# Optimization experiments

Measured on AMD Instinct MI355X. Metric: run time of the kernel, lower is better.

## Reference

```python
import jax, jax.numpy as jnp
import numpy as np

B, D, H, L = 65536, 784, 392, 32

def _lin(x, W, b):
    return x @ W.T + b

def setup_inputs() -> dict:
    key = jax.random.key(0)
    ks = jax.random.split(key, 10)
    def w(k, shape):
        fan_in = shape[1]
        return jax.random.normal(k, shape, jnp.float32) * (1.0 / np.sqrt(fan_in))
    return {
        'x': jax.random.uniform(ks[0], (B, D), jnp.float32),
        'eps_z': jax.random.normal(ks[1], (B, L), jnp.float32),
        'eps_y': jax.random.normal(ks[2], (B, D), jnp.float32),
        'W_e1': w(ks[3], (H, D)), 'b_e1': jnp.zeros((H,), jnp.float32),
        'W_emu': w(ks[4], (L, H)), 'b_emu': jnp.zeros((L,), jnp.float32),
        'W_elv': w(ks[5], (L, H)), 'b_elv': jnp.zeros((L,), jnp.float32),
        'W_d1': w(ks[6], (H, L)), 'b_d1': jnp.zeros((H,), jnp.float32),
        'W_dmu': w(ks[7], (D, H)), 'b_dmu': jnp.zeros((D,), jnp.float32),
        'W_dlv': w(ks[8], (D, H)), 'b_dlv': jnp.zeros((D,), jnp.float32),
    }

def reference(x, eps_z, eps_y, W_e1, b_e1, W_emu, b_emu, W_elv, b_elv,
              W_d1, b_d1, W_dmu, b_dmu, W_dlv, b_dlv):
    # encode
    h = jax.nn.relu(_lin(x, W_e1, b_e1))
    mu_z = jax.nn.relu(_lin(h, W_emu, b_emu))
    logvar_z = jax.nn.relu(_lin(h, W_elv, b_elv))
    # reparameterize
    z = mu_z + eps_z * jnp.exp(0.5 * logvar_z)
    # decode
    hd = jax.nn.relu(_lin(z, W_d1, b_d1))
    mu_y = jax.nn.relu(_lin(hd, W_dmu, b_dmu))
    logvar_y = jax.nn.relu(_lin(hd, W_dlv, b_dlv))
    image_res = jax.nn.sigmoid(mu_y + eps_y * jnp.exp(0.5 * logvar_y))
    # NLL: MultivariateNormal(mu, cov=diag(exp(0.5*logvar))).log_prob(x), closed form
    # (original looped per-sample with a Cholesky of a diag matrix; math identical)
    d = mu_y.shape[1]
    var = jnp.exp(0.5 * logvar_y)            # diagonal covariance entries
    quad = jnp.sum((x - mu_y) ** 2 / var, axis=1)
    logdet = jnp.sum(0.5 * logvar_y, axis=1)
    log_prob = -0.5 * (d * jnp.log(2.0 * jnp.pi) + logdet + quad)
    nll = -jnp.mean(log_prob)
    # KL regularisation, faithful to source formula incl. log(1e-8 + exp(logvar))
    kl = jnp.sum(0.5 * jnp.sum(mu_z ** 2 + jnp.exp(logvar_z)
                               - jnp.log(1e-8 + jnp.exp(logvar_z)) - 1.0, axis=1))
    return image_res, nll + kl
```

## Files before the change

### kernel.cpp

```cpp
#include <hip/hip_runtime.h>

#define B_N   65536
#define D_N   784
#define H_N   392
#define L_N   32
#define OUT_IMG ((size_t)B_N * D_N)

#define M_ROWS 64
#define HSTR   392

typedef unsigned short ushort_t;
typedef __attribute__((ext_vector_type(8))) short short8;
typedef __attribute__((ext_vector_type(4))) float f32x4;

#define N_WE1  358400
#define N_WEZ  26624
#define N_WD1  13312
#define N_WDY  745472
#define N_W16  (N_WE1 + N_WEZ + N_WD1 + N_WDY)
#define N_BIAS 2720
#define WS_BYTES (N_W16*2 + N_BIAS*4)

__device__ __forceinline__ unsigned short f2bf(float f) {
  union { float f; unsigned u; } v; v.f = f;
  unsigned r = v.u + 0x7FFFu + ((v.u >> 16) & 1u);
  return (unsigned short)(r >> 16);
}

__device__ __forceinline__ void gl2lds16(const void* g, void* l) {
  __builtin_amdgcn_global_load_lds(
      (const __attribute__((address_space(1))) unsigned int*)(unsigned long long)g,
      (__attribute__((address_space(3))) unsigned int*)(unsigned int)(unsigned long long)l,
      16, 0, 0);
}

__global__ void vae_prep(const float* __restrict__ We1, const float* __restrict__ Wemu,
                         const float* __restrict__ Welv, const float* __restrict__ Wd1,
                         const float* __restrict__ Wdmu, const float* __restrict__ Wdlv,
                         const float* __restrict__ be1, const float* __restrict__ bemu,
                         const float* __restrict__ belv, const float* __restrict__ bd1,
                         const float* __restrict__ bdmu, const float* __restrict__ bdlv,
                         ushort_t* __restrict__ ws16, float* __restrict__ wsb,
                         float* __restrict__ scalar_out) {
  int idx = blockIdx.x * 256 + threadIdx.x;
  if (idx == 0) *scalar_out = 0.f;
  if (idx < N_W16) {
    float val;
    if (idx < N_WE1) {
      int e = idx; int j = e & 7, lane = (e >> 3) & 63, g = e >> 9;
      int nt = g % 28, kt = g / 28;
      int n = nt * 16 + (lane & 15), k = kt * 32 + ((lane >> 4) << 3) + j;
      val = (n < H_N && k < D_N) ? We1[n * D_N + k] : 0.f;
    } else if (idx < N_WE1 + N_WEZ) {
      int e = idx - N_WE1; int j = e & 7, lane = (e >> 3) & 63, g = e >> 9;
      int kt = g % 13, nt = g / 13;
      int n = nt * 16 + (lane & 15), k = kt * 32 + ((lane >> 4) << 3) + j;
      val = (k < H_N) ? (n < 32 ? Wemu[n * H_N + k] : Welv[(n - 32) * H_N + k]) : 0.f;
    } else if (idx < N_WE1 + N_WEZ + N_WD1) {
      int e = idx - N_WE1 - N_WEZ; int j = e & 7, lane = (e >> 3) & 63, nt = e >> 9;
      int n = nt * 16 + (lane & 15), k = ((lane >> 4) << 3) + j;
      val = (n < H_N) ? Wd1[n * L_N + k] : 0.f;
    } else {
      int e = idx - N_WE1 - N_WEZ - N_WD1; int j = e & 7, lane = (e >> 3) & 63, g = e >> 9;
      int tt = g & 3, nw = (g >> 2) & 3, c = (g >> 4) % 7, kt = g / 112;
      int pair = nw * 14 + 2 * c + (tt >> 1);
      int d = pair * 16 + (lane & 15);
      int k = kt * 32 + ((lane >> 4) << 3) + j;
      val = (d < D_N && k < H_N) ? ((tt & 1) ? Wdlv[d * H_N + k] : Wdmu[d * H_N + k]) : 0.f;
    }
    ws16[idx] = f2bf(val);
  } else {
    int bi = idx - N_W16;
    if (bi < N_BIAS) {
      float val;
      if      (bi < 448)  val = (bi < H_N) ? be1[bi] : 0.f;
      else if (bi < 512)  { int i2 = bi - 448;  val = (i2 < 32) ? bemu[i2] : belv[i2 - 32]; }
      else if (bi < 928)  { int i2 = bi - 512;  val = (i2 < H_N) ? bd1[i2] : 0.f; }
      else if (bi < 1824) { int i2 = bi - 928;  val = (i2 < D_N) ? bdmu[i2] : 0.f; }
      else                { int i2 = bi - 1824; val = (i2 < D_N) ? bdlv[i2] : 0.f; }
      wsb[bi] = val;
    }
  }
}

__global__ __launch_bounds__(512, 4) void vae_main(
    const float* __restrict__ x, const float* __restrict__ eps_z,
    const float* __restrict__ eps_y,
    const ushort_t* __restrict__ ws16, const float* __restrict__ wsb,
    float* __restrict__ out, float* __restrict__ scalar_out) {
  const ushort_t* We1t = ws16;
  const ushort_t* Wezt = ws16 + N_WE1;
  const ushort_t* Wd1t = Wezt + N_WEZ;
  const ushort_t* Wdyt = Wd1t + N_WD1;
  const float* be1p  = wsb;
  const float* bezp  = wsb + 448;
  const float* bd1p  = wsb + 512;
  const float* bdmup = wsb + 928;
  const float* bdlvp = wsb + 1824;

  __shared__ __align__(16) ushort_t hbuf[M_ROWS * HSTR + 32];
  __shared__ __align__(16) ushort_t wslab[28 * 512];
  __shared__ float red[8];

  ushort_t* zb = wslab;

  const int tid  = threadIdx.x;
  const int w    = tid >> 6;
  const int lane = tid & 63;
  const int quad = lane >> 4;
  const int l16  = lane & 15;
  const int mw   = w >> 2, nw = w & 3;
  const int rb   = blockIdx.x * M_ROWS;

  float kl_acc = 0.f, q_acc = 0.f, ld_acc = 0.f;

  if (tid < 32) hbuf[M_ROWS * HSTR + tid] = 0;

  f32x4 acc1[2][7];
  {
    f32x4 z4 = {0.f, 0.f, 0.f, 0.f};
#pragma unroll
    for (int i = 0; i < 2; ++i)
#pragma unroll
      for (int t = 0; t < 7; ++t) acc1[i][t] = z4;
  }
  const float* xp[2];
#pragma unroll
  for (int i = 0; i < 2; ++i)
    xp[i] = x + (size_t)(rb + mw * 32 + i * 16 + l16) * D_N + quad * 8;

  for (int kt = 0; kt < 25; ++kt) {
    __syncthreads();
#pragma unroll
    for (int i = 0; i < 4; ++i) {
      int g = i * 512 + tid;
      if (g < 1792) gl2lds16((const char*)We1t + kt * 28672 + g * 16, (char*)wslab + g * 16);
    }
    short8 afr[2];
    {
      bool real = !(kt == 24 && quad >= 2);
#pragma unroll
      for (int i = 0; i < 2; ++i) {
        union { int4 p; short8 s; } u;
        if (real) {
          const float4* px = (const float4*)(xp[i] + kt * 32);
          float4 v0 = px[0], v1 = px[1];
          u.p.x = f2bf(v0.x) | ((unsigned)f2bf(v0.y) << 16);
          u.p.y = f2bf(v0.z) | ((unsigned)f2bf(v0.w) << 16);
          u.p.z = f2bf(v1.x) | ((unsigned)f2bf(v1.y) << 16);
          u.p.w = f2bf(v1.z) | ((unsigned)f2bf(v1.w) << 16);
        } else {
          u.p.x = 0; u.p.y = 0; u.p.z = 0; u.p.w = 0;
        }
        afr[i] = u.s;
      }
    }
    __syncthreads();
    __builtin_amdgcn_s_setprio(1);
#pragma unroll
    for (int t = 0; t < 7; ++t) {
      short8 bfr = *(const short8*)(wslab + ((nw * 7 + t) * 64 + lane) * 8);
#pragma unroll
      for (int i = 0; i < 2; ++i)
        acc1[i][t] = __builtin_amdgcn_mfma_f32_16x16x32_bf16(afr[i], bfr, acc1[i][t], 0, 0, 0);
    }
    __builtin_amdgcn_s_setprio(0);
  }
#pragma unroll
  for (int t = 0; t < 7; ++t) {
    int ntg = nw * 7 + t;
    if (ntg < 25) {
      int n = ntg * 16 + l16;
      bool ok = (n < H_N);
      float bb = ok ? be1p[n] : 0.f;
#pragma unroll
      for (int i = 0; i < 2; ++i)
#pragma unroll
        for (int r = 0; r < 4; ++r) {
          int m = mw * 32 + i * 16 + quad * 4 + r;
          if (ok) hbuf[m * HSTR + n] = f2bf(fmaxf(acc1[i][t][r] + bb, 0.f));
        }
    }
  }
  __syncthreads();

  if (w < 4) {
    f32x4 acc2[4];
    {
      f32x4 z4 = {0.f, 0.f, 0.f, 0.f};
#pragma unroll
      for (int nt = 0; nt < 4; ++nt) acc2[nt] = z4;
    }
    for (int kt = 0; kt < 13; ++kt) {
      short8 a = *(const short8*)(hbuf + (16 * w + l16) * HSTR + kt * 32 + quad * 8);
#pragma unroll
      for (int nt = 0; nt < 4; ++nt) {
        short8 b = *(const short8*)(Wezt + ((nt * 13 + kt) * 64 + lane) * 8);
        acc2[nt] = __builtin_amdgcn_mfma_f32_16x16x32_bf16(a, b, acc2[nt], 0, 0, 0);
      }
    }
#pragma unroll
    for (int s = 0; s < 2; ++s) {
      float bmu = bezp[s * 16 + l16];
      float blv = bezp[32 + s * 16 + l16];
#pragma unroll
      for (int r = 0; r < 4; ++r) {
        float mu = fmaxf(acc2[s][r] + bmu, 0.f);
        float lv = fmaxf(acc2[s + 2][r] + blv, 0.f);
        int m = 16 * w + quad * 4 + r;
        int gm = rb + m;
        int l = s * 16 + l16;
        float e = __expf(lv);
        kl_acc += 0.5f * (mu * mu + e - __logf(1e-8f + e) - 1.f);
        float zz = mu + eps_z[gm * 32 + l] * __expf(0.5f * lv);
        zb[m * 40 + l] = f2bf(zz);
      }
    }
  }
  __syncthreads();

  {
    const int rw = (w & 3) * 16;
    const int wh = w >> 2;
    short8 az = *(const short8*)(zb + (rw + l16) * 40 + quad * 8);
    for (int t2 = 0; t2 < 13; ++t2) {
      int nt = wh * 13 + t2;
      if (nt >= 25) continue;
      short8 b = *(const short8*)(Wd1t + (nt * 64 + lane) * 8);
      f32x4 a4 = {0.f, 0.f, 0.f, 0.f};
      a4 = __builtin_amdgcn_mfma_f32_16x16x32_bf16(az, b, a4, 0, 0, 0);
      int n = nt * 16 + l16;
      bool ok = (n < H_N);
      float bb = ok ? bd1p[n] : 0.f;
#pragma unroll
      for (int r = 0; r < 4; ++r) {
        int m = rw + quad * 4 + r;
        if (ok) hbuf[m * HSTR + n] = f2bf(fmaxf(a4[r] + bb, 0.f));
      }
    }
  }
  __syncthreads();

  for (int c = 0; c < 7; ++c) {
    f32x4 acc5[2][4];
    {
      f32x4 z4 = {0.f, 0.f, 0.f, 0.f};
#pragma unroll
      for (int i = 0; i < 2; ++i)
#pragma unroll
        for (int tt = 0; tt < 4; ++tt) acc5[i][tt] = z4;
    }
    for (int kt = 0; kt < 13; ++kt) {
      __syncthreads();
#pragma unroll
      for (int i = 0; i < 2; ++i) {
        int g = i * 512 + tid;
        gl2lds16((const char*)Wdyt + (kt * 7 + c) * 16384 + g * 16, (char*)wslab + g * 16);
      }
      __syncthreads();
      short8 a[2];
#pragma unroll
      for (int i = 0; i < 2; ++i)
        a[i] = *(const short8*)(hbuf + (mw * 32 + i * 16 + l16) * HSTR + kt * 32 + quad * 8);
      __builtin_amdgcn_s_setprio(1);
#pragma unroll
      for (int tt = 0; tt < 4; ++tt) {
        short8 b = *(const short8*)(wslab + ((nw * 4 + tt) * 64 + lane) * 8);
#pragma unroll
        for (int i = 0; i < 2; ++i)
          acc5[i][tt] = __builtin_amdgcn_mfma_f32_16x16x32_bf16(a[i], b, acc5[i][tt], 0, 0, 0);
      }
      __builtin_amdgcn_s_setprio(0);
    }
#pragma unroll
    for (int s = 0; s < 2; ++s) {
      int d = (nw * 14 + 2 * c + s) * 16 + l16;
      if (d < D_N) {
        float bmu = bdmup[d], blv = bdlvp[d];
#pragma unroll
        for (int i = 0; i < 2; ++i) {
#pragma unroll
          for (int r = 0; r < 4; ++r) {
            int m = mw * 32 + i * 16 + quad * 4 + r;
            size_t gi = (size_t)(rb + m) * D_N + d;
            float mu = fmaxf(acc5[i][2 * s][r] + bmu, 0.f);
            float lv = fmaxf(acc5[i][2 * s + 1][r] + blv, 0.f);
            float sd = __expf(0.5f * lv);
            float ey = __builtin_nontemporal_load(&eps_y[gi]);
            float xx = __builtin_nontemporal_load(&x[gi]);
            float tval = mu + ey * sd;
            __builtin_nontemporal_store(__builtin_amdgcn_rcpf(1.f + __expf(-tval)), &out[gi]);
            float dq = xx - mu;
            q_acc  += dq * dq * __builtin_amdgcn_rcpf(sd);
            ld_acc += 0.5f * lv;
          }
        }
      }
    }
  }

  float v = (0.5f / (float)B_N) * (ld_acc + q_acc) + kl_acc;
#pragma unroll
  for (int off = 32; off; off >>= 1) v += __shfl_down(v, off, 64);
  if (lane == 0) red[w] = v;
  __syncthreads();
  if (tid == 0) {
    float tot = 0.f;
#pragma unroll
    for (int i = 0; i < 8; ++i) tot += red[i];
    if (blockIdx.x == 0) tot += 720.447808f;
    atomicAdd(scalar_out, tot);
  }
}

extern "C" void kernel_launch(void* const* d_in, const int* in_sizes, int n_in,
                              void* d_out, int out_size, void* d_ws, size_t ws_size,
                              hipStream_t stream) {
  const float* x     = (const float*)d_in[0];
  const float* eps_z = (const float*)d_in[1];
  const float* eps_y = (const float*)d_in[2];
  const float* We1   = (const float*)d_in[3];
  const float* be1   = (const float*)d_in[4];
  const float* Wemu  = (const float*)d_in[5];
  const float* bemu  = (const float*)d_in[6];
  const float* Welv  = (const float*)d_in[7];
  const float* belv  = (const float*)d_in[8];
  const float* Wd1   = (const float*)d_in[9];
  const float* bd1   = (const float*)d_in[10];
  const float* Wdmu  = (const float*)d_in[11];
  const float* bdmu  = (const float*)d_in[12];
  const float* Wdlv  = (const float*)d_in[13];
  const float* bdlv  = (const float*)d_in[14];

  float* out = (float*)d_out;
  float* scalar_out = out + OUT_IMG;

  ushort_t* ws16 = (ushort_t*)d_ws;
  float* wsb = (float*)((char*)d_ws + (size_t)N_W16 * 2);

  int prep_total = N_W16 + N_BIAS;
  int prep_blocks = (prep_total + 255) / 256;
  vae_prep<<<prep_blocks, 256, 0, stream>>>(We1, Wemu, Welv, Wd1, Wdmu, Wdlv,
                                            be1, bemu, belv, bd1, bdmu, bdlv,
                                            ws16, wsb, scalar_out);

  vae_main<<<B_N / M_ROWS, 512, 0, stream>>>(x, eps_z, eps_y, ws16, wsb, out, scalar_out);
}
```

Baseline: 735.2 us.

## Load MFMA weight fragments directly from global instead of staging through LDS

Removes the LDS weight slab and the global_load_lds staging in both the encoder-1 and decoder-output GEMM loops. Each wave now reads its B fragments straight from the pre-swizzled global weight buffer, which drops two __syncthreads per k-step and frees LDS for higher occupancy. The last encoder k-tile is peeled out so the main loop carries no padding branch, and the loops are unrolled by two. The cost is redundant per-wave global/L2 weight traffic, since the two M-waves now fetch the same weights separately, plus load latency that is no longer hidden behind LDS.

After: 1.219 ms. 65.9% more time.

```diff
diff --git a/kernel.cpp b/kernel.cpp
--- a/kernel.cpp
+++ b/kernel.cpp
@@ -25,13 +25,6 @@
   union { float f; unsigned u; } v; v.f = f;
   unsigned r = v.u + 0x7FFFu + ((v.u >> 16) & 1u);
   return (unsigned short)(r >> 16);
-}
-
-__device__ __forceinline__ void gl2lds16(const void* g, void* l) {
-  __builtin_amdgcn_global_load_lds(
-      (const __attribute__((address_space(1))) unsigned int*)(unsigned long long)g,
-      (__attribute__((address_space(3))) unsigned int*)(unsigned int)(unsigned long long)l,
-      16, 0, 0);
 }
 
 __global__ void vae_prep(const float* __restrict__ We1, const float* __restrict__ Wemu,
@@ -99,10 +92,8 @@
   const float* bdlvp = wsb + 1824;
 
   __shared__ __align__(16) ushort_t hbuf[M_ROWS * HSTR + 32];
-  __shared__ __align__(16) ushort_t wslab[28 * 512];
+  __shared__ __align__(16) ushort_t zbuf[M_ROWS * 40];
   __shared__ float red[8];
-
-  ushort_t* zb = wslab;
 
   const int tid  = threadIdx.x;
   const int w    = tid >> 6;
@@ -129,42 +120,54 @@
   for (int i = 0; i < 2; ++i)
     xp[i] = x + (size_t)(rb + mw * 32 + i * 16 + l16) * D_N + quad * 8;
 
-  for (int kt = 0; kt < 25; ++kt) {
-    __syncthreads();
-#pragma unroll
-    for (int i = 0; i < 4; ++i) {
-      int g = i * 512 + tid;
-      if (g < 1792) gl2lds16((const char*)We1t + kt * 28672 + g * 16, (char*)wslab + g * 16);
-    }
+#pragma unroll 2
+  for (int kt = 0; kt < 24; ++kt) {
     short8 afr[2];
-    {
-      bool real = !(kt == 24 && quad >= 2);
-#pragma unroll
-      for (int i = 0; i < 2; ++i) {
-        union { int4 p; short8 s; } u;
-        if (real) {
-          const float4* px = (const float4*)(xp[i] + kt * 32);
-          float4 v0 = px[0], v1 = px[1];
-          u.p.x = f2bf(v0.x) | ((unsigned)f2bf(v0.y) << 16);
-          u.p.y = f2bf(v0.z) | ((unsigned)f2bf(v0.w) << 16);
-          u.p.z = f2bf(v1.x) | ((unsigned)f2bf(v1.y) << 16);
-          u.p.w = f2bf(v1.z) | ((unsigned)f2bf(v1.w) << 16);
-        } else {
-          u.p.x = 0; u.p.y = 0; u.p.z = 0; u.p.w = 0;
-        }
-        afr[i] = u.s;
-      }
-    }
-    __syncthreads();
+#pragma unroll
+    for (int i = 0; i < 2; ++i) {
+      const float4* px = (const float4*)(xp[i] + kt * 32);
+      float4 v0 = px[0], v1 = px[1];
+      union { int4 p; short8 s; } u;
+      u.p.x = f2bf(v0.x) | ((unsigned)f2bf(v0.y) << 16);
+      u.p.y = f2bf(v0.z) | ((unsigned)f2bf(v0.w) << 16);
+      u.p.z = f2bf(v1.x) | ((unsigned)f2bf(v1.y) << 16);
+      u.p.w = f2bf(v1.z) | ((unsigned)f2bf(v1.w) << 16);
+      afr[i] = u.s;
+    }
     __builtin_amdgcn_s_setprio(1);
 #pragma unroll
     for (int t = 0; t < 7; ++t) {
-      short8 bfr = *(const short8*)(wslab + ((nw * 7 + t) * 64 + lane) * 8);
+      short8 bfr = *(const short8*)(We1t + ((kt * 28 + nw * 7 + t) * 64 + lane) * 8);
 #pragma unroll
       for (int i = 0; i < 2; ++i)
         acc1[i][t] = __builtin_amdgcn_mfma_f32_16x16x32_bf16(afr[i], bfr, acc1[i][t], 0, 0, 0);
     }
     __builtin_amdgcn_s_setprio(0);
+  }
+  {
+    short8 afr[2];
+#pragma unroll
+    for (int i = 0; i < 2; ++i) {
+      union { int4 p; short8 s; } u;
+      if (quad < 2) {
+        const float4* px = (const float4*)(xp[i] + 24 * 32);
+        float4 v0 = px[0], v1 = px[1];
+        u.p.x = f2bf(v0.x) | ((unsigned)f2bf(v0.y) << 16);
+        u.p.y = f2bf(v0.z) | ((unsigned)f2bf(v0.w) << 16);
+        u.p.z = f2bf(v1.x) | ((unsigned)f2bf(v1.y) << 16);
+        u.p.w = f2bf(v1.z) | ((unsigned)f2bf(v1.w) << 16);
+      } else {
+        u.p.x = 0; u.p.y = 0; u.p.z = 0; u.p.w = 0;
+      }
+      afr[i] = u.s;
+    }
+#pragma unroll
+    for (int t = 0; t < 7; ++t) {
+      short8 bfr = *(const short8*)(We1t + ((24 * 28 + nw * 7 + t) * 64 + lane) * 8);
+#pragma unroll
+      for (int i = 0; i < 2; ++i)
+        acc1[i][t] = __builtin_amdgcn_mfma_f32_16x16x32_bf16(afr[i], bfr, acc1[i][t], 0, 0, 0);
+    }
   }
 #pragma unroll
   for (int t = 0; t < 7; ++t) {
@@ -213,7 +216,7 @@
         float e = __expf(lv);
         kl_acc += 0.5f * (mu * mu + e - __logf(1e-8f + e) - 1.f);
         float zz = mu + eps_z[gm * 32 + l] * __expf(0.5f * lv);
-        zb[m * 40 + l] = f2bf(zz);
+        zbuf[m * 40 + l] = f2bf(zz);
       }
     }
   }
@@ -222,7 +225,7 @@
   {
     const int rw = (w & 3) * 16;
     const int wh = w >> 2;
-    short8 az = *(const short8*)(zb + (rw + l16) * 40 + quad * 8);
+    short8 az = *(const short8*)(zbuf + (rw + l16) * 40 + quad * 8);
     for (int t2 = 0; t2 < 13; ++t2) {
       int nt = wh * 13 + t2;
       if (nt >= 25) continue;
@@ -250,26 +253,21 @@
 #pragma unroll
         for (int tt = 0; tt < 4; ++tt) acc5[i][tt] = z4;
     }
+#pragma unroll 2
     for (int kt = 0; kt < 13; ++kt) {
-      __syncthreads();
-#pragma unroll
-      for (int i = 0; i < 2; ++i) {
-        int g = i * 512 + tid;
-        gl2lds16((const char*)Wdyt + (kt * 7 + c) * 16384 + g * 16, (char*)wslab + g * 16);
-      }
-      __syncthreads();
-      short8 a[2];
+      short8 a[2], b[4];
 #pragma unroll
       for (int i = 0; i < 2; ++i)
         a[i] = *(const short8*)(hbuf + (mw * 32 + i * 16 + l16) * HSTR + kt * 32 + quad * 8);
+#pragma unroll
+      for (int tt = 0; tt < 4; ++tt)
+        b[tt] = *(const short8*)(Wdyt + ((kt * 112 + c * 16 + nw * 4 + tt) * 64 + lane) * 8);
       __builtin_amdgcn_s_setprio(1);
 #pragma unroll
-      for (int tt = 0; tt < 4; ++tt) {
-        short8 b = *(const short8*)(wslab + ((nw * 4 + tt) * 64 + lane) * 8);
+      for (int tt = 0; tt < 4; ++tt)
 #pragma unroll
         for (int i = 0; i < 2; ++i)
-          acc5[i][tt] = __builtin_amdgcn_mfma_f32_16x16x32_bf16(a[i], b, acc5[i][tt], 0, 0, 0);
-      }
+          acc5[i][tt] = __builtin_amdgcn_mfma_f32_16x16x32_bf16(a[i], b[tt], acc5[i][tt], 0, 0, 0);
       __builtin_amdgcn_s_setprio(0);
     }
 #pragma unroll
```
